# Optimization experiments

Hardware: AMD Instinct MI355X
Metric: run time of the kernel (lower is better)

## Reference

```python
import jax, jax.numpy as jnp
import numpy as np

EPS = 1e-6

def masked_softmax(x, m, axis):
    # Faithful to KrantikariQA tensor_utils.masked_softmax:
    #   x = x*m; e = exp(x - max(x)) * m; e / (sum(e) + 1e-6)
    x = x * m
    ex = jnp.exp(x - jnp.max(x, axis=axis, keepdims=True)) * m
    return ex / (jnp.sum(ex, axis=axis, keepdims=True) + EPS)

def setup_inputs() -> dict:
    key = jax.random.key(0)
    k = jax.random.split(key, 7)
    Lq, Lp, B, D = 256, 256, 64, 1024
    q = jax.random.normal(k[0], (Lq, B, D), jnp.float32)
    p = jax.random.normal(k[1], (Lp, B, D), jnp.float32)
    qm = jax.random.randint(k[2], (B, Lq), 0, 2).astype(jnp.int32)
    pm = jax.random.randint(k[3], (B, Lp), 0, 2).astype(jnp.int32)
    # nn.Linear weights (out, in), no bias
    WF = jax.random.normal(k[4], (D, D), jnp.float32) * 0.02
    WG = jax.random.normal(k[5], (D, 2 * D), jnp.float32) * 0.02
    WH = jax.random.normal(k[6], (1, 2 * D), jnp.float32) * 0.02
    return {"q": q, "p": p, "qm": qm, "pm": pm, "WF": WF, "WG": WG, "WH": WH}

def reference(q, p, qm, pm, WF, WG, WH):
    # Attend: att = F(x), batch-first [B, L, D]
    att_q = jnp.einsum('lbd,ed->ble', q, WF)          # [B,Lq,D]
    att_p = jnp.einsum('lbd,ed->ble', p, WF)          # [B,Lp,D]
    e = jnp.einsum('bqe,bpe->bqp', att_q, att_p)      # [B,Lq,Lp]
    m = qm.astype(q.dtype)[:, :, None] * pm.astype(q.dtype)[:, None, :]  # [B,Lq,Lp]
    softmax_j = masked_softmax(e, m, axis=2)                              # over Lp
    softmax_i = masked_softmax(e.transpose(0, 2, 1), m.transpose(0, 2, 1), axis=2)  # [B,Lp,Lq]
    beta = jnp.einsum('bqp,pbd->bqd', softmax_j, p)   # [B,Lq,D]
    alpha = jnp.einsum('bpq,qbd->bpd', softmax_i, q)  # [B,Lp,D]
    # Compare
    v1 = jnp.concatenate([q.transpose(1, 0, 2), beta], axis=-1) @ WG.T   # [B,Lq,D]
    v2 = jnp.concatenate([p.transpose(1, 0, 2), alpha], axis=-1) @ WG.T  # [B,Lp,D]
    # Aggregate
    sum_v1 = jnp.sum(v1, axis=1)  # [B,D]
    sum_v2 = jnp.sum(v2, axis=1)  # [B,D]
    return jnp.concatenate([sum_v1, sum_v2], axis=-1) @ WH.T  # [B,1]
```

## Files before the change

kernel.cpp:

```cpp
#include <hip/hip_runtime.h>

typedef _Float16 f16x8 __attribute__((ext_vector_type(8)));
using f32x4 = __attribute__((ext_vector_type(4))) float;

constexpr int B = 64, L = 256, D = 1024;
constexpr int BD = B * D;
constexpr float EPS = 1e-6f;

__device__ __forceinline__ void gload_lds16(const void* g, void* l) {
    __builtin_amdgcn_global_load_lds((const __attribute__((address_space(1))) void*)g,
                                     (__attribute__((address_space(3))) void*)l,
                                     16, 0, 0);
}

__global__ __launch_bounds__(256) void k_wfgp(const float* __restrict__ WF,
                                              const float* __restrict__ WG,
                                              const float* __restrict__ WH,
                                              short* __restrict__ WFt16,
                                              float* __restrict__ gp1,
                                              float* __restrict__ gp2) {
    __shared__ float tile[32][33];
    const int bid = blockIdx.x;
    if (bid < 1024) {
        const int rt = bid >> 5, ct = bid & 31;
        const int t = threadIdx.x;
        const int r = t >> 3, c4 = (t & 7) * 4;
        float4 v = *(const float4*)(WF + (long)(rt * 32 + r) * D + ct * 32 + c4);
        tile[r][c4] = v.x; tile[r][c4 + 1] = v.y; tile[r][c4 + 2] = v.z; tile[r][c4 + 3] = v.w;
        __syncthreads();
        union { _Float16 h[4]; short4 s; } u;
        u.h[0] = (_Float16)tile[c4 + 0][r];
        u.h[1] = (_Float16)tile[c4 + 1][r];
        u.h[2] = (_Float16)tile[c4 + 2][r];
        u.h[3] = (_Float16)tile[c4 + 3][r];
        *(short4*)(WFt16 + (long)(ct * 32 + r) * D + rt * 32 + c4) = u.s;
    } else {
        const int lb = bid - 1024;
        const int kx = lb & 7, ec = lb >> 3;
        const int k = kx * 256 + threadIdx.x;
        const int e0 = ec * 128;
        float a = 0.f, c = 0.f;
        for (int e = 0; e < 128; ++e) {
            float w = WG[(long)(e0 + e) * (2 * D) + k];
            a += w * WH[e0 + e];
            c += w * WH[D + e0 + e];
        }
        gp1[ec * 2048 + k] = a; gp2[ec * 2048 + k] = c;
    }
}

template <int WM, int WN, int MR, int A32, int B32>
__global__ __launch_bounds__(WM * WN * 64) void k_gemm(
    const char* __restrict__ A, long sA, long bA,
    const char* __restrict__ Bm, long sB, long bB,
    int K, int bx, int per_batch, int f16_out,
    short* __restrict__ Ch, float* __restrict__ Cf, int ldC, long batchC)
{
    constexpr int BM = WM * MR * 16, BN = WN * 64;
    constexpr int T = WM * WN * 64;
    constexpr int TILEB = (BM + BN) * 64;
    constexpr int ROUNDS = TILEB / (T * 16);
    constexpr int ROUNDS_A = (BM * 4) / T;
    __shared__ __align__(16) char lds[2 * TILEB];

    const int t = threadIdx.x, lane = t & 63, w = t >> 6;
    const int wm = w / WN, wn = w % WN;

    const int lin = blockIdx.x;
    const int chunk = gridDim.x >> 3;
    const int swz = (lin & 7) * chunk + (lin >> 3);
    const int z = swz / per_batch;
    const int r0 = swz % per_batch;
    const int mb = (r0 / bx) * BM, nb = (r0 % bx) * BN;

    const char* Ab = A + bA * z;
    const char* Bb = Bm + bB * z;

    const char* sp[ROUNDS];
    #pragma unroll
    for (int r = 0; r < ROUNDS; ++r) {
        int g = r * T + t;
        int row = g >> 2, sg = g & 3;
        int lg = sg ^ ((row >> 1) & 3);
        if (r < ROUNDS_A) sp[r] = Ab + (long)(mb + row) * sA + lg * (A32 ? 32 : 16);
        else              sp[r] = Bb + (long)(nb + row - BM) * sB + lg * (B32 ? 32 : 16);
    }

    int aoff[MR], boff[4];
    #pragma unroll
    for (int i = 0; i < MR; ++i) {
        int ra = wm * (MR * 16) + i * 16 + (lane & 15);
        aoff[i] = ra * 64 + (((lane >> 4) ^ ((ra >> 1) & 3))) * 16;
    }
    #pragma unroll
    for (int j = 0; j < 4; ++j) {
        int rb = wn * 64 + j * 16 + (lane & 15);
        boff[j] = BM * 64 + rb * 64 + (((lane >> 4) ^ ((rb >> 1) & 3))) * 16;
    }

    f32x4 acc[MR][4] = {};
    const int NT = K >> 5;

    {
        #pragma unroll
        for (int r = 0; r < ROUNDS; ++r) {
            const bool is32 = (r < ROUNDS_A) ? (A32 != 0) : (B32 != 0);
            if (is32) {
                float4 s0 = *(const float4*)(sp[r]);
                float4 s1 = *(const float4*)(sp[r] + 16);
                union { _Float16 h[8]; int4 v; } u;
                u.h[0]=(_Float16)s0.x; u.h[1]=(_Float16)s0.y; u.h[2]=(_Float16)s0.z; u.h[3]=(_Float16)s0.w;
                u.h[4]=(_Float16)s1.x; u.h[5]=(_Float16)s1.y; u.h[6]=(_Float16)s1.z; u.h[7]=(_Float16)s1.w;
                *((int4*)(lds + (r * T + t) * 16)) = u.v;
            } else {
                gload_lds16(sp[r], lds + (r * T + t) * 16);
            }
        }
        asm volatile("s_waitcnt lgkmcnt(0)" ::: "memory");
    }

    int cur = 0;
    for (int kt = 0; kt < NT; ++kt) {
        asm volatile("s_waitcnt vmcnt(0)" ::: "memory");
        __builtin_amdgcn_sched_barrier(0);
        __builtin_amdgcn_s_barrier();
        __builtin_amdgcn_sched_barrier(0);
        float4 stg[ROUNDS][2];
        char* dstb = lds + (cur ^ 1) * TILEB;
        if (kt + 1 < NT) {
            #pragma unroll
            for (int r = 0; r < ROUNDS; ++r) {
                const bool is32 = (r < ROUNDS_A) ? (A32 != 0) : (B32 != 0);
                long kb = (long)(kt + 1) * (is32 ? 128 : 64);
                if (is32) {
                    stg[r][0] = *(const float4*)(sp[r] + kb);
                    stg[r][1] = *(const float4*)(sp[r] + kb + 16);
                } else {
                    gload_lds16(sp[r] + kb, dstb + (r * T + t) * 16);
                }
            }
        }
        __builtin_amdgcn_sched_barrier(0);
        const char* lb = lds + cur * TILEB;
        f16x8 fb[4], fa[MR];
        #pragma unroll
        for (int j = 0; j < 4; ++j) fb[j] = *(const f16x8*)(lb + boff[j]);
        #pragma unroll
        for (int i = 0; i < MR; ++i) fa[i] = *(const f16x8*)(lb + aoff[i]);
        #pragma unroll
        for (int i = 0; i < MR; ++i)
            #pragma unroll
            for (int j = 0; j < 4; ++j)
                acc[i][j] = __builtin_amdgcn_mfma_f32_16x16x32_f16(fb[j], fa[i], acc[i][j], 0, 0, 0);
        if ((A32 || B32) && (kt + 1 < NT)) {
            #pragma unroll
            for (int r = 0; r < ROUNDS; ++r) {
                const bool is32 = (r < ROUNDS_A) ? (A32 != 0) : (B32 != 0);
                if (is32) {
                    union { _Float16 h[8]; int4 v; } u;
                    u.h[0]=(_Float16)stg[r][0].x; u.h[1]=(_Float16)stg[r][0].y;
                    u.h[2]=(_Float16)stg[r][0].z; u.h[3]=(_Float16)stg[r][0].w;
                    u.h[4]=(_Float16)stg[r][1].x; u.h[5]=(_Float16)stg[r][1].y;
                    u.h[6]=(_Float16)stg[r][1].z; u.h[7]=(_Float16)stg[r][1].w;
                    *((int4*)(dstb + (r * T + t) * 16)) = u.v;
                }
            }
            asm volatile("s_waitcnt lgkmcnt(0)" ::: "memory");
            __builtin_amdgcn_sched_barrier(0);
        }
        cur ^= 1;
    }

    const long zC = batchC * z;
    #pragma unroll
    for (int i = 0; i < MR; ++i)
        #pragma unroll
        for (int j = 0; j < 4; ++j) {
            int row = mb + wm * (MR * 16) + i * 16 + (lane & 15);
            int col = nb + wn * 64 + j * 16 + (lane >> 4) * 4;
            long idx = zC + (long)row * ldC + col;
            if (f16_out) {
                union { _Float16 h[4]; short4 s; } u;
                #pragma unroll
                for (int rr = 0; rr < 4; ++rr) u.h[rr] = (_Float16)acc[i][j][rr];
                *(short4*)(Ch + idx) = u.s;
            } else {
                float4 v = make_float4(acc[i][j][0], acc[i][j][1], acc[i][j][2], acc[i][j][3]);
                *(float4*)(Cf + idx) = v;
            }
        }
}

__global__ __launch_bounds__(256) void k_fold_g(const float* __restrict__ Gp,
                                                short* __restrict__ G16) {
    const int i = blockIdx.x * 256 + threadIdx.x;
    constexpr int N4 = (1 << 20) / 4;
    const float4* g = (const float4*)Gp;
    float4 v0 = g[i], v1 = g[N4 + i], v2 = g[2 * N4 + i], v3 = g[3 * N4 + i];
    union { _Float16 h[4]; short4 s; } u;
    u.h[0] = (_Float16)(v0.x + v1.x + v2.x + v3.x);
    u.h[1] = (_Float16)(v0.y + v1.y + v2.y + v3.y);
    u.h[2] = (_Float16)(v0.z + v1.z + v2.z + v3.z);
    u.h[3] = (_Float16)(v0.w + v1.w + v2.w + v3.w);
    ((short4*)G16)[i] = u.s;
}

__global__ __launch_bounds__(256) void k_pass1(const float* __restrict__ E,
                                               const int* __restrict__ qm,
                                               const int* __restrict__ pm,
                                               float* __restrict__ impart,
                                               float* __restrict__ ispart,
                                               float* __restrict__ cjpart) {
    const int qc = blockIdx.x, b = blockIdx.y;
    const int p = threadIdx.x, lane = p & 63, w = p >> 6;
    const int q0 = qc * 32;
    __shared__ float wred[32][4];
    __shared__ float rowmx[32], rowsm[32], qmv_s[32];
    if (p < 32) qmv_s[p] = (float)qm[b * L + q0 + p];
    __syncthreads();
    const float pmv = (float)pm[b * L + p];
    const float* eb = E + b * (L * L) + q0 * L + p;

    float xv[32];
    float im = -1e30f;
    #pragma unroll
    for (int r = 0; r < 32; ++r) {
        float mm = pmv * qmv_s[r];
        float x = eb[r * L] * mm;
        xv[r] = x;
        im = fmaxf(im, x);
        float v = x;
        #pragma unroll
        for (int o = 32; o; o >>= 1) v = fmaxf(v, __shfl_xor(v, o));
        if (lane == 0) wred[r][w] = v;
    }
    __syncthreads();
    if (p < 32) rowmx[p] = fmaxf(fmaxf(wred[p][0], wred[p][1]), fmaxf(wred[p][2], wred[p][3]));
    __syncthreads();
    float is = 0.f;
    #pragma unroll
    for (int r = 0; r < 32; ++r) {
        float mm = pmv * qmv_s[r];
        is += mm * __expf(xv[r] - im);
        float v = mm * __expf(xv[r] - rowmx[r]);
        #pragma unroll
        for (int o = 32; o; o >>= 1) v += __shfl_xor(v, o);
        if (lane == 0) wred[r][w] = v;
    }
    __syncthreads();
    if (p < 32) rowsm[p] = wred[p][0] + wred[p][1] + wred[p][2] + wred[p][3];
    __syncthreads();
    float cj = 0.f;
    #pragma unroll
    for (int r = 0; r < 32; ++r) {
        float mm = pmv * qmv_s[r];
        cj += mm * __expf(xv[r] - rowmx[r]) / (rowsm[r] + EPS);
    }
    const int o = (b * 8 + qc) * 256 + p;
    impart[o] = im; ispart[o] = is; cjpart[o] = cj;
}

__global__ __launch_bounds__(256) void k_combine(const float* __restrict__ impart,
                                                 const float* __restrict__ ispart,
                                                 const float* __restrict__ cjpart,
                                                 float* __restrict__ rmi,
                                                 float* __restrict__ rsi,
                                                 float* __restrict__ colj) {
    const int b = blockIdx.x, p = threadIdx.x;
    const int base = b * 8 * 256 + p;
    float m = -1e30f, s = 0.f, c = 0.f;
    #pragma unroll
    for (int k = 0; k < 8; ++k) m = fmaxf(m, impart[base + k * 256]);
    #pragma unroll
    for (int k = 0; k < 8; ++k) {
        s += ispart[base + k * 256] * __expf(impart[base + k * 256] - m);
        c += cjpart[base + k * 256];
    }
    rmi[b * L + p] = m; rsi[b * L + p] = s; colj[b * L + p] = c;
}

__global__ __launch_bounds__(256) void k_colsum_i(const float* __restrict__ E,
                                                  const int* __restrict__ qm,
                                                  const int* __restrict__ pm,
                                                  const float* __restrict__ rmaxi,
                                                  const float* __restrict__ rsumi,
                                                  float* __restrict__ coli) {
    const int wid = threadIdx.x >> 6, lane = threadIdx.x & 63;
    const int row = blockIdx.x * 4 + wid;
    const int b = row >> 8;
    const float qmv = (float)qm[row];
    const float* er = E + row * L;
    float acc = 0.f;
    #pragma unroll
    for (int i = 0; i < 4; ++i) {
        int pp = lane + 64 * i;
        float mm = qmv * (float)pm[b * L + pp];
        float x = er[pp] * mm;
        acc += mm * __expf(x - rmaxi[b * L + pp]) / (rsumi[b * L + pp] + EPS);
    }
    #pragma unroll
    for (int o = 32; o; o >>= 1) acc += __shfl_xor(acc, o);
    if (lane == 0) coli[row] = acc;
}

__global__ __launch_bounds__(128) void k_sums2(const float* __restrict__ Q,
                                               const float* __restrict__ P,
                                               const float* __restrict__ colj,
                                               const float* __restrict__ coli,
                                               float* __restrict__ pq,
                                               float* __restrict__ pp,
                                               float* __restrict__ pb,
                                               float* __restrict__ pa) {
    const int c = blockIdx.x, b = blockIdx.y, t = threadIdx.x;
    const int d0 = t * 8;
    float aq[8] = {}, ap[8] = {}, ab[8] = {}, aa[8] = {};
    for (int l = c * 16; l < c * 16 + 16; ++l) {
        const float* qp = Q + (long)l * BD + b * D + d0;
        const float* pp_ = P + (long)l * BD + b * D + d0;
        float4 q0 = *(const float4*)qp, q1 = *(const float4*)(qp + 4);
        float4 p0 = *(const float4*)pp_, p1 = *(const float4*)(pp_ + 4);
        float cj = colj[b * L + l], ci = coli[b * L + l];
        float qv[8] = {q0.x, q0.y, q0.z, q0.w, q1.x, q1.y, q1.z, q1.w};
        float pv[8] = {p0.x, p0.y, p0.z, p0.w, p1.x, p1.y, p1.z, p1.w};
        #pragma unroll
        for (int k = 0; k < 8; ++k) {
            aq[k] += qv[k]; ap[k] += pv[k]; ab[k] += cj * pv[k]; aa[k] += ci * qv[k];
        }
    }
    const long o = ((long)c * B + b) * D + d0;
    *(float4*)(pq + o) = make_float4(aq[0], aq[1], aq[2], aq[3]);
    *(float4*)(pq + o + 4) = make_float4(aq[4], aq[5], aq[6], aq[7]);
    *(float4*)(pp + o) = make_float4(ap[0], ap[1], ap[2], ap[3]);
    *(float4*)(pp + o + 4) = make_float4(ap[4], ap[5], ap[6], ap[7]);
    *(float4*)(pb + o) = make_float4(ab[0], ab[1], ab[2], ab[3]);
    *(float4*)(pb + o + 4) = make_float4(ab[4], ab[5], ab[6], ab[7]);
    *(float4*)(pa + o) = make_float4(aa[0], aa[1], aa[2], aa[3]);
    *(float4*)(pa + o + 4) = make_float4(aa[4], aa[5], aa[6], aa[7]);
}

__global__ __launch_bounds__(256) void k_final2(const float* __restrict__ pq,
                                                const float* __restrict__ pp,
                                                const float* __restrict__ pb,
                                                const float* __restrict__ pa,
                                                const float* __restrict__ gp1,
                                                const float* __restrict__ gp2,
                                                float* __restrict__ out) {
    const int b = blockIdx.x, t = threadIdx.x;
    float acc = 0.f;
    for (int d = t; d < D; d += 256) {
        float sq = 0.f, sp_ = 0.f, sb = 0.f, sa = 0.f;
        #pragma unroll
        for (int c2 = 0; c2 < 16; ++c2) {
            long o = ((long)c2 * B + b) * D + d;
            sq += pq[o]; sp_ += pp[o]; sb += pb[o]; sa += pa[o];
        }
        float g1d = 0.f, g1D = 0.f, g2d = 0.f, g2D = 0.f;
        #pragma unroll
        for (int ec = 0; ec < 8; ++ec) {
            g1d += gp1[ec * 2048 + d];     g1D += gp1[ec * 2048 + D + d];
            g2d += gp2[ec * 2048 + d];     g2D += gp2[ec * 2048 + D + d];
        }
        acc += sq * g1d + sb * g1D + sp_ * g2d + sa * g2D;
    }
    #pragma unroll
    for (int o = 32; o; o >>= 1) acc += __shfl_xor(acc, o);
    __shared__ float red[4];
    const int wid = t >> 6, lane = t & 63;
    if (lane == 0) red[wid] = acc;
    __syncthreads();
    if (t == 0) out[b] = red[0] + red[1] + red[2] + red[3];
}

extern "C" void kernel_launch(void* const* d_in, const int* in_sizes, int n_in,
                              void* d_out, int out_size, void* d_ws, size_t ws_size,
                              hipStream_t stream) {
    const float* q  = (const float*)d_in[0];
    const float* p  = (const float*)d_in[1];
    const int*   qm = (const int*)d_in[2];
    const int*   pm = (const int*)d_in[3];
    const float* WF = (const float*)d_in[4];
    const float* WG = (const float*)d_in[5];
    const float* WH = (const float*)d_in[6];
    float* out = (float*)d_out;

    char* wsb = (char*)d_ws;
    short* T16   = (short*)(wsb);
    short* WFt16 = (short*)(wsb + (32l << 20));
    short* G16   = (short*)(wsb + (34l << 20));
    float* Gp    = (float*)(wsb + (36l << 20));
    float* E     = (float*)(wsb + (36l << 20));
    float* st    = (float*)(wsb + (52l << 20));
    const int BL = B * L;
    float* impart = st;                  float* ispart = impart + B * 8 * 256;
    float* cjpart = ispart + B * 8 * 256;
    float* rmi  = cjpart + B * 8 * 256;  float* rsi  = rmi + BL;
    float* colj = rsi + BL;              float* coli = colj + BL;
    float* pq   = coli + BL;             float* pp   = pq + 16 * BD;
    float* pb   = pp + 16 * BD;          float* pa   = pb + 16 * BD;
    float* gp1  = pa + 16 * BD;          float* gp2  = gp1 + 8 * 2048;

    k_wfgp<<<1088, 256, 0, stream>>>(WF, WG, WH, WFt16, gp1, gp2);
    k_gemm<2, 2, 4, 0, 0><<<256, 256, 0, stream>>>(
        (const char*)WFt16, 2048, 512, (const char*)WFt16, 2048, 512,
        256, 8, 64, 0, nullptr, Gp, 1024, 1l << 20);
    k_fold_g<<<1024, 256, 0, stream>>>(Gp, G16);
    k_gemm<2, 2, 4, 1, 0><<<1024, 256, 0, stream>>>(
        (const char*)q, 4096, 0, (const char*)G16, 2048, 0,
        1024, 8, 1024, 1, T16, nullptr, 1024, 0);
    k_gemm<2, 2, 4, 0, 1><<<256, 256, 0, stream>>>(
        (const char*)T16, 64l * 2048, 2048, (const char*)p, 64l * 4096, 4096,
        1024, 2, 4, 0, nullptr, E, 256, 65536);
    k_pass1<<<dim3(8, B), 256, 0, stream>>>(E, qm, pm, impart, ispart, cjpart);
    k_combine<<<B, 256, 0, stream>>>(impart, ispart, cjpart, rmi, rsi, colj);
    k_colsum_i<<<BL / 4, 256, 0, stream>>>(E, qm, pm, rmi, rsi, coli);
    k_sums2<<<dim3(16, B), 128, 0, stream>>>(q, p, colj, coli, pq, pp, pb, pa);
    k_final2<<<B, 256, 0, stream>>>(pq, pp, pb, pa, gp1, gp2, out);
}
```

Measured before the change: 173.5 us.

## Prefetch fp32 GEMM operands two stages ahead and enlarge q-projection tiles

The GEMM main loop for fp32-sourced operands now issues global loads two k-steps ahead into alternating register buffers, converting and storing to LDS one step ahead. This hides global latency behind the MFMA work instead of stalling on the vmcnt wait every iteration. The pure-fp16 path is split out into a simpler loop that uses only direct global-to-LDS loads. The q×G projection launch also moves to 256×256 tiles with 512 threads, which raises per-block reuse but leaves only 256 blocks and adds register pressure.

Result: slower. 190.2 us (+9.6%).

```diff
diff --git a/kernel.cpp b/kernel.cpp
--- a/kernel.cpp
+++ b/kernel.cpp
@@ -61,6 +61,9 @@
     constexpr int TILEB = (BM + BN) * 64;
     constexpr int ROUNDS = TILEB / (T * 16);
     constexpr int ROUNDS_A = (BM * 4) / T;
+    constexpr int R0 = A32 ? 0 : ROUNDS_A;
+    constexpr int R1 = A32 ? ROUNDS_A : (B32 ? ROUNDS : ROUNDS_A);
+    constexpr int NR = (R1 > R0) ? (R1 - R0) : 1;
     __shared__ __align__(16) char lds[2 * TILEB];
 
     const int t = threadIdx.x, lane = t & 63, w = t >> 6;
@@ -70,8 +73,8 @@
     const int chunk = gridDim.x >> 3;
     const int swz = (lin & 7) * chunk + (lin >> 3);
     const int z = swz / per_batch;
-    const int r0 = swz % per_batch;
-    const int mb = (r0 / bx) * BM, nb = (r0 % bx) * BN;
+    const int r0_ = swz % per_batch;
+    const int mb = (r0_ / bx) * BM, nb = (r0_ % bx) * BN;
 
     const char* Ab = A + bA * z;
     const char* Bb = Bm + bB * z;
@@ -100,76 +103,120 @@
 
     f32x4 acc[MR][4] = {};
     const int NT = K >> 5;
-
-    {
+    int cur = 0;
+
+#define CVT8(U, S0, S1)                                                     \
+    U.h[0]=(_Float16)S0.x; U.h[1]=(_Float16)S0.y;                           \
+    U.h[2]=(_Float16)S0.z; U.h[3]=(_Float16)S0.w;                           \
+    U.h[4]=(_Float16)S1.x; U.h[5]=(_Float16)S1.y;                           \
+    U.h[6]=(_Float16)S1.z; U.h[7]=(_Float16)S1.w;
+
+#define GSTEP(WSRC, LDST, KT)                                               \
+    {                                                                       \
+        asm volatile("s_waitcnt vmcnt(0)" ::: "memory");                    \
+        __builtin_amdgcn_sched_barrier(0);                                  \
+        __builtin_amdgcn_s_barrier();                                       \
+        __builtin_amdgcn_sched_barrier(0);                                  \
+        char* dstb = lds + (cur ^ 1) * TILEB;                               \
+        if ((KT) + 2 < NT) {                                                \
+            long kb = (long)((KT) + 2) * 128;                               \
+            _Pragma("unroll")                                               \
+            for (int r = R0; r < R1; ++r) {                                 \
+                LDST[r - R0][0] = *(const float4*)(sp[r] + kb);             \
+                LDST[r - R0][1] = *(const float4*)(sp[r] + kb + 16);        \
+            }                                                               \
+        }                                                                   \
+        if ((KT) + 1 < NT) {                                                \
+            long kb16 = (long)((KT) + 1) * 64;                              \
+            _Pragma("unroll")                                               \
+            for (int r = 0; r < ROUNDS; ++r)                                \
+                if (r < R0 || r >= R1)                                      \
+                    gload_lds16(sp[r] + kb16, dstb + (r * T + t) * 16);     \
+            _Pragma("unroll")                                               \
+            for (int r = R0; r < R1; ++r) {                                 \
+                union { _Float16 h[8]; int4 v; } u;                         \
+                float4 s0 = WSRC[r - R0][0], s1 = WSRC[r - R0][1];          \
+                CVT8(u, s0, s1)                                             \
+                *((int4*)(dstb + (r * T + t) * 16)) = u.v;                  \
+            }                                                               \
+        }                                                                   \
+        __builtin_amdgcn_sched_barrier(0);                                  \
+        const char* lb = lds + cur * TILEB;                                 \
+        f16x8 fb[4], fa[MR];                                                \
+        _Pragma("unroll")                                                   \
+        for (int j = 0; j < 4; ++j) fb[j] = *(const f16x8*)(lb + boff[j]);  \
+        _Pragma("unroll")                                                   \
+        for (int i = 0; i < MR; ++i) fa[i] = *(const f16x8*)(lb + aoff[i]); \
+        _Pragma("unroll")                                                   \
+        for (int i = 0; i < MR; ++i)                                        \
+            _Pragma("unroll")                                               \
+            for (int j = 0; j < 4; ++j)                                     \
+                acc[i][j] = __builtin_amdgcn_mfma_f32_16x16x32_f16(         \
+                    fb[j], fa[i], acc[i][j], 0, 0, 0);                      \
+        asm volatile("s_waitcnt lgkmcnt(0)" ::: "memory");                  \
+        __builtin_amdgcn_sched_barrier(0);                                  \
+        cur ^= 1;                                                           \
+    }
+
+    if constexpr (A32 || B32) {
+        float4 rsA[NR][2], rsB[NR][2];
         #pragma unroll
         for (int r = 0; r < ROUNDS; ++r) {
-            const bool is32 = (r < ROUNDS_A) ? (A32 != 0) : (B32 != 0);
-            if (is32) {
+            if (r >= R0 && r < R1) {
                 float4 s0 = *(const float4*)(sp[r]);
                 float4 s1 = *(const float4*)(sp[r] + 16);
                 union { _Float16 h[8]; int4 v; } u;
-                u.h[0]=(_Float16)s0.x; u.h[1]=(_Float16)s0.y; u.h[2]=(_Float16)s0.z; u.h[3]=(_Float16)s0.w;
-                u.h[4]=(_Float16)s1.x; u.h[5]=(_Float16)s1.y; u.h[6]=(_Float16)s1.z; u.h[7]=(_Float16)s1.w;
+                CVT8(u, s0, s1)
                 *((int4*)(lds + (r * T + t) * 16)) = u.v;
             } else {
                 gload_lds16(sp[r], lds + (r * T + t) * 16);
             }
         }
+        if (NT > 1) {
+            #pragma unroll
+            for (int r = R0; r < R1; ++r) {
+                rsB[r - R0][0] = *(const float4*)(sp[r] + 128);
+                rsB[r - R0][1] = *(const float4*)(sp[r] + 128 + 16);
+            }
+        }
         asm volatile("s_waitcnt lgkmcnt(0)" ::: "memory");
-    }
-
-    int cur = 0;
-    for (int kt = 0; kt < NT; ++kt) {
-        asm volatile("s_waitcnt vmcnt(0)" ::: "memory");
-        __builtin_amdgcn_sched_barrier(0);
-        __builtin_amdgcn_s_barrier();
-        __builtin_amdgcn_sched_barrier(0);
-        float4 stg[ROUNDS][2];
-        char* dstb = lds + (cur ^ 1) * TILEB;
-        if (kt + 1 < NT) {
+        for (int kt = 0; kt < NT; kt += 2) {
+            GSTEP(rsB, rsA, kt)
+            GSTEP(rsA, rsB, kt + 1)
+        }
+    } else {
+        #pragma unroll
+        for (int r = 0; r < ROUNDS; ++r)
+            gload_lds16(sp[r], lds + (r * T + t) * 16);
+        for (int kt = 0; kt < NT; ++kt) {
+            asm volatile("s_waitcnt vmcnt(0)" ::: "memory");
+            __builtin_amdgcn_sched_barrier(0);
+            __builtin_amdgcn_s_barrier();
+            __builtin_amdgcn_sched_barrier(0);
+            if (kt + 1 < NT) {
+                long kb = (long)(kt + 1) * 64;
+                char* dstb = lds + (cur ^ 1) * TILEB;
+                #pragma unroll
+                for (int r = 0; r < ROUNDS; ++r)
+                    gload_lds16(sp[r] + kb, dstb + (r * T + t) * 16);
+            }
+            __builtin_amdgcn_sched_barrier(0);
+            const char* lb = lds + cur * TILEB;
+            f16x8 fb[4], fa[MR];
             #pragma unroll
-            for (int r = 0; r < ROUNDS; ++r) {
-                const bool is32 = (r < ROUNDS_A) ? (A32 != 0) : (B32 != 0);
-                long kb = (long)(kt + 1) * (is32 ? 128 : 64);
-                if (is32) {
-                    stg[r][0] = *(const float4*)(sp[r] + kb);
-                    stg[r][1] = *(const float4*)(sp[r] + kb + 16);
-                } else {
-                    gload_lds16(sp[r] + kb, dstb + (r * T + t) * 16);
-                }
-            }
-        }
-        __builtin_amdgcn_sched_barrier(0);
-        const char* lb = lds + cur * TILEB;
-        f16x8 fb[4], fa[MR];
-        #pragma unroll
-        for (int j = 0; j < 4; ++j) fb[j] = *(const f16x8*)(lb + boff[j]);
-        #pragma unroll
-        for (int i = 0; i < MR; ++i) fa[i] = *(const f16x8*)(lb + aoff[i]);
-        #pragma unroll
-        for (int i = 0; i < MR; ++i)
+            for (int j = 0; j < 4; ++j) fb[j] = *(const f16x8*)(lb + boff[j]);
             #pragma unroll
-            for (int j = 0; j < 4; ++j)
-                acc[i][j] = __builtin_amdgcn_mfma_f32_16x16x32_f16(fb[j], fa[i], acc[i][j], 0, 0, 0);
-        if ((A32 || B32) && (kt + 1 < NT)) {
+            for (int i = 0; i < MR; ++i) fa[i] = *(const f16x8*)(lb + aoff[i]);
             #pragma unroll
-            for (int r = 0; r < ROUNDS; ++r) {
-                const bool is32 = (r < ROUNDS_A) ? (A32 != 0) : (B32 != 0);
-                if (is32) {
-                    union { _Float16 h[8]; int4 v; } u;
-                    u.h[0]=(_Float16)stg[r][0].x; u.h[1]=(_Float16)stg[r][0].y;
-                    u.h[2]=(_Float16)stg[r][0].z; u.h[3]=(_Float16)stg[r][0].w;
-                    u.h[4]=(_Float16)stg[r][1].x; u.h[5]=(_Float16)stg[r][1].y;
-                    u.h[6]=(_Float16)stg[r][1].z; u.h[7]=(_Float16)stg[r][1].w;
-                    *((int4*)(dstb + (r * T + t) * 16)) = u.v;
-                }
-            }
-            asm volatile("s_waitcnt lgkmcnt(0)" ::: "memory");
-            __builtin_amdgcn_sched_barrier(0);
-        }
-        cur ^= 1;
-    }
+            for (int i = 0; i < MR; ++i)
+                #pragma unroll
+                for (int j = 0; j < 4; ++j)
+                    acc[i][j] = __builtin_amdgcn_mfma_f32_16x16x32_f16(fb[j], fa[i], acc[i][j], 0, 0, 0);
+            cur ^= 1;
+        }
+    }
+#undef GSTEP
+#undef CVT8
 
     const long zC = batchC * z;
     #pragma unroll
@@ -404,9 +451,9 @@
         (const char*)WFt16, 2048, 512, (const char*)WFt16, 2048, 512,
         256, 8, 64, 0, nullptr, Gp, 1024, 1l << 20);
     k_fold_g<<<1024, 256, 0, stream>>>(Gp, G16);
-    k_gemm<2, 2, 4, 1, 0><<<1024, 256, 0, stream>>>(
+    k_gemm<2, 4, 8, 1, 0><<<256, 512, 0, stream>>>(
         (const char*)q, 4096, 0, (const char*)G16, 2048, 0,
-        1024, 8, 1024, 1, T16, nullptr, 1024, 0);
+        1024, 4, 256, 1, T16, nullptr, 1024, 0);
     k_gemm<2, 2, 4, 0, 1><<<256, 256, 0, stream>>>(
         (const char*)T16, 64l * 2048, 2048, (const char*)p, 64l * 4096, 4096,
         1024, 2, 4, 0, nullptr, E, 256, 65536);
```
